# Optimization experiments

Hardware: AMD Instinct MI355X
Metric: run time of the kernel (lower is better)

## Reference

```python
import jax, jax.numpy as jnp
import numpy as np

RMAX = 5.0   # max_radius
NB = 8       # bessel bases
NSH = 9      # (lmax+1)^2, lmax=2
S = 4        # message passing steps


def _rms(x):
    return x * jax.lax.rsqrt(jnp.mean(x * x, axis=-1, keepdims=True) + 1e-6)


def _mlp(x, w1, b1, w2, b2):
    # 2-layer MLP (base_mlp_depth=2) with silu activation + rms_norm output
    return _rms(jax.nn.silu(x @ w1 + b1) @ w2 + b2)


def _sh(u):
    # real spherical harmonics up to l=2, component normalization (e3nn style), u: [E,3] unit vectors
    x, y, z = u[:, 0], u[:, 1], u[:, 2]
    s3, s5, s15 = 3.0 ** 0.5, 5.0 ** 0.5, 15.0 ** 0.5
    return jnp.stack([
        jnp.ones_like(x),
        s3 * x, s3 * y, s3 * z,
        s15 * x * y, s15 * y * z, 0.5 * s5 * (3.0 * z * z - 1.0),
        s15 * x * z, 0.5 * s15 * (x * x - y * y)], axis=1)


def setup_inputs() -> dict:
    key = jax.random.key(0)
    ks = iter(jax.random.split(key, 64))
    N, E, D, H, L, BOND = 20000, 640000, 128, 256, 128, 16

    def w(shape, fan):
        return jax.random.normal(next(ks), shape, jnp.float32) / np.float32(np.sqrt(fan))

    return dict(
        pos=jax.random.normal(next(ks), (N, 3), jnp.float32),
        c_in=jnp.ones((1,), jnp.float32),
        atom_type_index=jax.random.randint(next(ks), (N,), 0, 20),
        atom_code_index=jax.random.randint(next(ks), (N,), 0, 10),
        residue_code_index=jax.random.randint(next(ks), (N,), 0, 25),
        residue_sequence_index=jnp.zeros((N,), jnp.int32),  # max_sequence_length=1
        senders=jax.random.randint(next(ks), (E,), 0, N),
        receivers=jax.random.randint(next(ks), (E,), 0, N),
        bond_mask=jax.random.randint(next(ks), (E,), 0, 2),
        emb_at=w((20, 32), 1.0), emb_ac=w((10, 32), 1.0),
        emb_rc=w((25, 32), 1.0), emb_ri=w((1, 32), 1.0),
        emb_bond=w((2, BOND), 1.0),
        nenc_w1=w((D, H), D), nenc_b1=jnp.zeros((H,), jnp.float32),
        nenc_w2=w((H, L), H), nenc_b2=jnp.zeros((L,), jnp.float32),
        eenc_w1=w((NB * NSH + BOND, H), NB * NSH + BOND), eenc_b1=jnp.zeros((H,), jnp.float32),
        eenc_w2=w((H, L), H), eenc_b2=jnp.zeros((L,), jnp.float32),
        msg_w1=w((S, 3 * L, H), 3 * L), msg_b1=jnp.zeros((S, H), jnp.float32),
        msg_w2=w((S, H, L), H), msg_b2=jnp.zeros((S, L), jnp.float32),
        gate_w=w((S, L, 1), L), gate_b=jnp.zeros((S, 1), jnp.float32),
        upd_w1=w((S, 2 * L, H), 2 * L), upd_b1=jnp.zeros((S, H), jnp.float32),
        upd_w2=w((S, H, L), H), upd_b2=jnp.zeros((S, L), jnp.float32),
        head_w1=w((L, H), L), head_b1=jnp.zeros((H,), jnp.float32),
        head_w2=w((H, 3), H), head_b2=jnp.zeros((3,), jnp.float32),
    )


def reference(pos, c_in, atom_type_index, atom_code_index, residue_code_index,
              residue_sequence_index, senders, receivers, bond_mask,
              emb_at, emb_ac, emb_rc, emb_ri, emb_bond,
              nenc_w1, nenc_b1, nenc_w2, nenc_b2,
              eenc_w1, eenc_b1, eenc_w2, eenc_b2,
              msg_w1, msg_b1, msg_w2, msg_b2, gate_w, gate_b,
              upd_w1, upd_b1, upd_w2, upd_b2,
              head_w1, head_b1, head_w2, head_b2):
    N = pos.shape[0]
    E = senders.shape[0]

    # --- update_features: embeddings + edge vectors ---
    node_emb = jnp.concatenate([
        emb_at[atom_type_index], emb_ac[atom_code_index],
        emb_rc[residue_code_index], emb_ri[residue_sequence_index]], axis=1)  # [N,128]
    bond_emb = emb_bond[bond_mask]                                            # [E,16]

    up = pos / c_in
    vec = up[senders] - up[receivers]                                         # [E,3]
    r = jnp.sqrt(jnp.sum(vec * vec, axis=-1) + 1e-12)                         # [E]
    u = vec / r[:, None]

    # Bessel RBF: sqrt(2/rmax) * sin(n*pi*r/rmax) / r
    n = jnp.arange(1, NB + 1, dtype=jnp.float32)
    rbf = jnp.sqrt(2.0 / RMAX) * jnp.sin(n[None, :] * jnp.pi * r[:, None] / RMAX) / r[:, None]
    # cosine distance cutoff envelope
    cut = 0.5 * (jnp.cos(jnp.pi * jnp.minimum(r, RMAX) / RMAX) + 1.0) * (r < RMAX)

    ylm = _sh(u)                                                              # [E,9]
    radial = (rbf[:, :, None] * ylm[:, None, :]).reshape(E, NB * NSH) * cut[:, None]

    # --- encoders ---
    h = _mlp(node_emb, nenc_w1, nenc_b1, nenc_w2, nenc_b2)                    # [N,L]
    e = _mlp(jnp.concatenate([radial, bond_emb], axis=1),
             eenc_w1, eenc_b1, eenc_w2, eenc_b2)                              # [E,L]

    # --- message passing: gather -> MLP -> sigmoid-gate * cutoff -> scatter ---
    for s in range(S):
        m = _mlp(jnp.concatenate([h[senders], h[receivers], e], axis=1),
                 msg_w1[s], msg_b1[s], msg_w2[s], msg_b2[s])                  # [E,L]
        g = jax.nn.sigmoid(m @ gate_w[s] + gate_b[s]) * cut[:, None]          # [E,1]
        agg = jax.ops.segment_sum(m * g, receivers, num_segments=N)           # [N,L]
        h = h + _mlp(jnp.concatenate([h, agg], axis=1),
                     upd_w1[s], upd_b1[s], upd_w2[s], upd_b2[s])
        e = e + m

    # --- head: predict per-node 3-vector ---
    return jax.nn.silu(h @ head_w1 + head_b1) @ head_w2 + head_b2             # [N,3]
```

## Files before the change

kernel.cpp:

```cpp
#include <hip/hip_runtime.h>
#include <hip/hip_bf16.h>
#include <math.h>


#define TILE   16
#define STRIDE 20

using short8 = __attribute__((ext_vector_type(8))) short;
using f32x4  = __attribute__((ext_vector_type(4))) float;

__device__ __forceinline__ float silu_f(float x) {
  return x / (1.0f + __expf(-x));
}
__device__ __forceinline__ unsigned short f2b(float x) {
  union { float f; unsigned u; } v; v.f = x;
  unsigned r = v.u + 0x7fffu + ((v.u >> 16) & 1u);
  return (unsigned short)(r >> 16);
}
__device__ __forceinline__ float b2f(unsigned short h) {
  union { unsigned u; float f; } v; v.u = ((unsigned)h) << 16;
  return v.f;
}

__global__ __launch_bounds__(256) void pack_w_kernel(
    const float* __restrict__ src, unsigned short* __restrict__ dst,
    int Kreal, int KS, int NF)
{
  const int N = NF * 16;
  const int total = NF * KS * 512;
  for (int idx = blockIdx.x * 256 + threadIdx.x; idx < total; idx += gridDim.x * 256) {
    const int nf  = idx / (KS * 512);
    const int rem = idx - nf * (KS * 512);
    const int kk  = rem >> 9;
    const int p   = rem & 511;
    const int l   = p >> 3, j = p & 7;
    const int c   = nf * 16 + (l & 15);
    const int k   = kk * 32 + ((l >> 4) << 3) + j;
    dst[idx] = (k < Kreal) ? f2b(src[(size_t)k * N + c]) : (unsigned short)0;
  }
}

template<int KS1>
__device__ __forceinline__ void mfma_l1_compute(const unsigned short* __restrict__ x1,
                                                const unsigned short* __restrict__ w1p,
                                                int tid, f32x4 acc[8])
{
  const int w  = tid >> 6;
  const int l  = tid & 63;
  const int lr = l & 15;
  const int lk = (l >> 4) << 3;
  const int RS = KS1 * 32;
  const f32x4 zz = {0.f, 0.f, 0.f, 0.f};
  #pragma unroll
  for (int i = 0; i < 8; ++i) acc[i] = zz;

  for (int kk = 0; kk < KS1; ++kk) {
    short8 af[2];
    #pragma unroll
    for (int mf = 0; mf < 2; ++mf) {
      const int r = mf * 16 + lr;
      const int k = kk * 32 + lk;
      af[mf] = *(const short8*)&x1[r * RS + ((((k >> 3) ^ (r & 7))) << 3)];
    }
    #pragma unroll
    for (int nf = 0; nf < 4; ++nf) {
      const int nfg = w * 4 + nf;
      const short8 bf = *(const short8*)&w1p[(size_t)(((nfg * KS1) + kk) * 64 + l) * 8];
      #pragma unroll
      for (int mf = 0; mf < 2; ++mf)
        acc[mf * 4 + nf] = __builtin_amdgcn_mfma_f32_16x16x32_bf16(af[mf], bf, acc[mf * 4 + nf], 0, 0, 0);
    }
  }
}

__device__ __forceinline__ void l1_store_silu(const f32x4 acc[8],
                                              const float* __restrict__ b1,
                                              unsigned short* __restrict__ hsm,
                                              int tid)
{
  const int w = tid >> 6, l = tid & 63, lr = l & 15;
  #pragma unroll
  for (int nf = 0; nf < 4; ++nf) {
    const int c = (w * 4 + nf) * 16 + lr;
    const float bias = b1[c];
    #pragma unroll
    for (int mf = 0; mf < 2; ++mf) {
      #pragma unroll
      for (int q = 0; q < 4; ++q) {
        const int r = mf * 16 + ((l >> 4) << 2) + q;
        const float v = silu_f(acc[mf * 4 + nf][q] + bias);
        hsm[r * 256 + (((c >> 3) ^ (r & 7)) << 3) + (c & 7)] = f2b(v);
      }
    }
  }
}

__device__ __forceinline__ void mfma_l2(const unsigned short* __restrict__ hsm,
                                        const unsigned short* __restrict__ w2p,
                                        const float* __restrict__ b2,
                                        int tid, f32x4 acc2[4])
{
  const int w  = tid >> 6;
  const int l  = tid & 63;
  const int lr = l & 15;
  const int lk = (l >> 4) << 3;
  const f32x4 zz = {0.f, 0.f, 0.f, 0.f};
  #pragma unroll
  for (int i = 0; i < 4; ++i) acc2[i] = zz;

  for (int kk = 0; kk < 8; ++kk) {
    short8 af[2];
    #pragma unroll
    for (int mf = 0; mf < 2; ++mf) {
      const int r = mf * 16 + lr;
      const int k = kk * 32 + lk;
      af[mf] = *(const short8*)&hsm[r * 256 + (((k >> 3) ^ (r & 7)) << 3)];
    }
    #pragma unroll
    for (int nf2 = 0; nf2 < 2; ++nf2) {
      const int nfg = w * 2 + nf2;
      const short8 bf = *(const short8*)&w2p[(size_t)(((nfg * 8) + kk) * 64 + l) * 8];
      #pragma unroll
      for (int mf = 0; mf < 2; ++mf)
        acc2[mf * 2 + nf2] = __builtin_amdgcn_mfma_f32_16x16x32_bf16(af[mf], bf, acc2[mf * 2 + nf2], 0, 0, 0);
    }
  }
  #pragma unroll
  for (int nf2 = 0; nf2 < 2; ++nf2) {
    const float bias = b2[(w * 2 + nf2) * 16 + lr];
    #pragma unroll
    for (int mf = 0; mf < 2; ++mf) {
      #pragma unroll
      for (int q = 0; q < 4; ++q) acc2[mf * 2 + nf2][q] += bias;
    }
  }
}

__device__ __forceinline__ void rms_reduce(const f32x4 acc2[4], float* rsum,
                                           int tid, float mval[2][2][4])
{
  const int l = tid & 63;
  #pragma unroll
  for (int mf = 0; mf < 2; ++mf) {
    #pragma unroll
    for (int q = 0; q < 4; ++q) {
      float s = acc2[mf * 2][q] * acc2[mf * 2][q]
              + acc2[mf * 2 + 1][q] * acc2[mf * 2 + 1][q];
      s += __shfl_xor(s, 1); s += __shfl_xor(s, 2);
      s += __shfl_xor(s, 4); s += __shfl_xor(s, 8);
      if ((l & 15) == 0)
        atomicAdd(&rsum[mf * 16 + ((l >> 4) << 2) + q], s);
    }
  }
  __syncthreads();
  #pragma unroll
  for (int mf = 0; mf < 2; ++mf) {
    #pragma unroll
    for (int q = 0; q < 4; ++q) {
      const int r = mf * 16 + ((l >> 4) << 2) + q;
      const float inv = rsqrtf(rsum[r] * (1.0f / 128.0f) + 1e-6f);
      #pragma unroll
      for (int nf2 = 0; nf2 < 2; ++nf2)
        mval[mf][nf2][q] = acc2[mf * 2 + nf2][q] * inv;
    }
  }
}

__global__ __launch_bounds__(256, 5) void edge_enc_mfma(
    const float* __restrict__ pos, const float* __restrict__ c_in,
    const int* __restrict__ snd, const int* __restrict__ rcv,
    const int* __restrict__ bnd, const float* __restrict__ embb,
    const unsigned short* __restrict__ w1p, const float* __restrict__ b1,
    const unsigned short* __restrict__ w2p, const float* __restrict__ b2,
    unsigned short* __restrict__ e_g, float* __restrict__ cutb, int E)
{
  __shared__ __align__(16) unsigned short smem[32 * 256];
  unsigned short* x1  = smem;
  unsigned short* hsm = smem;
  __shared__ float grbf[32][8];
  __shared__ float gylm[32][9];
  __shared__ float gcut[32];
  __shared__ int   gbond[32];
  __shared__ float rsum[32];
  const int tid = threadIdx.x;
  const int e0  = blockIdx.x * 32;

  if (tid < 32) {
    rsum[tid] = 0.f;
    const int ed = min(e0 + tid, E - 1);
    const int sa = snd[ed], ra = rcv[ed];
    const float ci = c_in[0];
    const float vx = (pos[sa * 3 + 0] - pos[ra * 3 + 0]) / ci;
    const float vy = (pos[sa * 3 + 1] - pos[ra * 3 + 1]) / ci;
    const float vz = (pos[sa * 3 + 2] - pos[ra * 3 + 2]) / ci;
    const float r  = sqrtf(vx * vx + vy * vy + vz * vz + 1e-12f);
    const float ir = 1.0f / r;
    const float ux = vx * ir, uy = vy * ir, uz = vz * ir;
    const float PI = 3.14159265358979323846f;
    const float pr = PI * r * 0.2f;
    const float c0 = 0.632455532033675866f;
    #pragma unroll
    for (int n = 0; n < 8; ++n)
      grbf[tid][n] = c0 * sinf((float)(n + 1) * pr) * ir;
    const float cv = 0.5f * (cosf(PI * fminf(r, 5.0f) * 0.2f) + 1.0f)
                   * (r < 5.0f ? 1.0f : 0.0f);
    gcut[tid] = cv;
    if (e0 + tid < E) cutb[e0 + tid] = cv;
    const float s3  = 1.7320508075688772f;
    const float s5  = 2.2360679774997896f;
    const float s15 = 3.8729833462074170f;
    gylm[tid][0] = 1.0f;
    gylm[tid][1] = s3 * ux; gylm[tid][2] = s3 * uy; gylm[tid][3] = s3 * uz;
    gylm[tid][4] = s15 * ux * uy; gylm[tid][5] = s15 * uy * uz;
    gylm[tid][6] = 0.5f * s5 * (3.0f * uz * uz - 1.0f);
    gylm[tid][7] = s15 * ux * uz;
    gylm[tid][8] = 0.5f * s15 * (ux * ux - uy * uy);
    gbond[tid] = bnd[ed];
  }
  __syncthreads();
  for (int i = tid; i < 32 * 16; i += 256) {
    const int r = i >> 4, g = i & 15;
    union { short8 v; unsigned short u[8]; } t;
    #pragma unroll
    for (int j = 0; j < 8; ++j) {
      const int k = g * 8 + j;
      float v;
      if (k < 72) { const int n = k / 9, mm = k - 9 * n; v = grbf[r][n] * gylm[r][mm] * gcut[r]; }
      else if (k < 88) v = embb[gbond[r] * 16 + (k - 72)];
      else v = 0.f;
      t.u[j] = f2b(v);
    }
    *(short8*)&x1[r * 128 + ((g ^ (r & 7)) << 3)] = t.v;
  }
  __syncthreads();
  f32x4 acc1[8];
  mfma_l1_compute<4>(x1, w1p, tid, acc1);
  __syncthreads();
  l1_store_silu(acc1, b1, hsm, tid);
  __syncthreads();
  f32x4 acc2[4];
  mfma_l2(hsm, w2p, b2, tid, acc2);
  float mval[2][2][4];
  rms_reduce(acc2, rsum, tid, mval);
  const int l = tid & 63, w = tid >> 6, lr = l & 15;
  #pragma unroll
  for (int mf = 0; mf < 2; ++mf) {
    #pragma unroll
    for (int q = 0; q < 4; ++q) {
      const int r = mf * 16 + ((l >> 4) << 2) + q;
      const int ed = e0 + r;
      if (ed < E) {
        #pragma unroll
        for (int nf2 = 0; nf2 < 2; ++nf2) {
          const int c2 = (w * 2 + nf2) * 16 + lr;
          e_g[(size_t)ed * 128 + c2] = f2b(mval[mf][nf2][q]);
        }
      }
    }
  }
}

__global__ __launch_bounds__(256, 5) void msg_mfma(
    const unsigned short* __restrict__ hb, unsigned short* __restrict__ e_g,
    float* __restrict__ agg, const float* __restrict__ cutb,
    const int* __restrict__ snd, const int* __restrict__ rcv,
    const unsigned short* __restrict__ w1p, const float* __restrict__ b1,
    const unsigned short* __restrict__ w2p, const float* __restrict__ b2,
    const float* __restrict__ gw, const float* __restrict__ gb, int E)
{
  __shared__ __align__(16) unsigned short smem[32 * 384];
  unsigned short* x1  = smem;
  unsigned short* hsm = smem;
  __shared__ int   snd_s[32], rcv_s[32];
  __shared__ float cut_s[32];
  __shared__ float rsum[32], gsum[32];
  const int tid = threadIdx.x;
  const int e0  = blockIdx.x * 32;

  if (tid < 32) {
    rsum[tid] = 0.f; gsum[tid] = 0.f;
    const int ed = min(e0 + tid, E - 1);
    snd_s[tid] = snd[ed]; rcv_s[tid] = rcv[ed]; cut_s[tid] = cutb[ed];
  }
  __syncthreads();
  for (int i = tid; i < 32 * 48; i += 256) {
    const int r = i / 48, g = i - r * 48;
    short8 t;
    if (g < 32) {
      const int node = (g < 16) ? snd_s[r] : rcv_s[r];
      t = *(const short8*)&hb[(size_t)node * 128 + (g & 15) * 8];
    } else {
      const int ed = min(e0 + r, E - 1);
      t = *(const short8*)&e_g[(size_t)ed * 128 + (g - 32) * 8];
    }
    *(short8*)&x1[r * 384 + ((g ^ (r & 7)) << 3)] = t;
  }
  __syncthreads();
  f32x4 acc1[8];
  mfma_l1_compute<12>(x1, w1p, tid, acc1);
  __syncthreads();
  l1_store_silu(acc1, b1, hsm, tid);
  __syncthreads();
  f32x4 acc2[4];
  mfma_l2(hsm, w2p, b2, tid, acc2);
  float mval[2][2][4];
  rms_reduce(acc2, rsum, tid, mval);

  const int l = tid & 63, w = tid >> 6, lr = l & 15;
  const float gw0 = gw[(w * 2 + 0) * 16 + lr];
  const float gw1 = gw[(w * 2 + 1) * 16 + lr];
  #pragma unroll
  for (int mf = 0; mf < 2; ++mf) {
    #pragma unroll
    for (int q = 0; q < 4; ++q) {
      float p = mval[mf][0][q] * gw0 + mval[mf][1][q] * gw1;
      p += __shfl_xor(p, 1); p += __shfl_xor(p, 2);
      p += __shfl_xor(p, 4); p += __shfl_xor(p, 8);
      if ((l & 15) == 0)
        atomicAdd(&gsum[mf * 16 + ((l >> 4) << 2) + q], p);
    }
  }
  __syncthreads();
  const float gbv = gb[0];
  #pragma unroll
  for (int mf = 0; mf < 2; ++mf) {
    #pragma unroll
    for (int q = 0; q < 4; ++q) {
      const int r = mf * 16 + ((l >> 4) << 2) + q;
      const int ed = e0 + r;
      if (ed < E) {
        const float gr = cut_s[r] / (1.0f + __expf(-(gsum[r] + gbv)));
        const int rv = rcv_s[r];
        #pragma unroll
        for (int nf2 = 0; nf2 < 2; ++nf2) {
          const int c2 = (w * 2 + nf2) * 16 + lr;
          const float m = mval[mf][nf2][q];
          const float eo = b2f(e_g[(size_t)ed * 128 + c2]);
          e_g[(size_t)ed * 128 + c2] = f2b(eo + m);
          atomicAdd(&agg[(size_t)rv * 128 + c2], m * gr);
        }
      }
    }
  }
}

__global__ __launch_bounds__(256, 5) void upd_mfma(
    float* __restrict__ h, unsigned short* __restrict__ hb,
    const float* __restrict__ agg,
    const unsigned short* __restrict__ w1p, const float* __restrict__ b1,
    const unsigned short* __restrict__ w2p, const float* __restrict__ b2,
    int N)
{
  __shared__ __align__(16) unsigned short smem[32 * 256];
  unsigned short* x1  = smem;
  unsigned short* hsm = smem;
  __shared__ float rsum[32];
  const int tid = threadIdx.x;
  const int n0  = blockIdx.x * 32;
  if (tid < 32) rsum[tid] = 0.f;
  __syncthreads();
  for (int i = tid; i < 32 * 32; i += 256) {
    const int r = i >> 5, g = i & 31;
    const int n = min(n0 + r, N - 1);
    short8 t;
    if (g < 16) {
      t = *(const short8*)&hb[(size_t)n * 128 + g * 8];
    } else {
      const float4 f0 = *(const float4*)&agg[(size_t)n * 128 + (g - 16) * 8];
      const float4 f1 = *(const float4*)&agg[(size_t)n * 128 + (g - 16) * 8 + 4];
      union { short8 v; unsigned short u[8]; } tt;
      tt.u[0] = f2b(f0.x); tt.u[1] = f2b(f0.y); tt.u[2] = f2b(f0.z); tt.u[3] = f2b(f0.w);
      tt.u[4] = f2b(f1.x); tt.u[5] = f2b(f1.y); tt.u[6] = f2b(f1.z); tt.u[7] = f2b(f1.w);
      t = tt.v;
    }
    *(short8*)&x1[r * 256 + ((g ^ (r & 7)) << 3)] = t;
  }
  __syncthreads();
  f32x4 acc1[8];
  mfma_l1_compute<8>(x1, w1p, tid, acc1);
  __syncthreads();
  l1_store_silu(acc1, b1, hsm, tid);
  __syncthreads();
  f32x4 acc2[4];
  mfma_l2(hsm, w2p, b2, tid, acc2);
  float mval[2][2][4];
  rms_reduce(acc2, rsum, tid, mval);
  const int l = tid & 63, w = tid >> 6, lr = l & 15;
  #pragma unroll
  for (int mf = 0; mf < 2; ++mf) {
    #pragma unroll
    for (int q = 0; q < 4; ++q) {
      const int r = mf * 16 + ((l >> 4) << 2) + q;
      const int n = n0 + r;
      if (n < N) {
        #pragma unroll
        for (int nf2 = 0; nf2 < 2; ++nf2) {
          const int c2 = (w * 2 + nf2) * 16 + lr;
          const float nh = h[(size_t)n * 128 + c2] + mval[mf][nf2][q];
          h[(size_t)n * 128 + c2]  = nh;
          hb[(size_t)n * 128 + c2] = f2b(nh);
        }
      }
    }
  }
}


__device__ __forceinline__ float loadE(const float* p)          { return *p; }
__device__ __forceinline__ float loadE(const __hip_bfloat16* p) { return __bfloat162float(*p); }
__device__ __forceinline__ void  storeE(float* p, float v)          { *p = v; }
__device__ __forceinline__ void  storeE(__hip_bfloat16* p, float v) { *p = __float2bfloat16(v); }

template<int K1>
__device__ __forceinline__ void layer1_silu(const float* __restrict__ xs,
                                            const float* __restrict__ w1,
                                            const float* __restrict__ b1,
                                            float* __restrict__ hs, int tid)
{
  const int jh = tid & 127;
  const int tp = tid >> 7;
  const int tbase = 8 * tp;
  float a[8] = {0,0,0,0,0,0,0,0};
  float b[8] = {0,0,0,0,0,0,0,0};
  const float* wp = w1 + jh;
  for (int k = 0; k < K1; ++k) {
    const float4 x0 = *(const float4*)&xs[k*STRIDE + tbase];
    const float4 x1 = *(const float4*)&xs[k*STRIDE + tbase + 4];
    const float wa = wp[k*256];
    const float wb = wp[k*256 + 128];
    a[0] = fmaf(x0.x, wa, a[0]); a[1] = fmaf(x0.y, wa, a[1]);
    a[2] = fmaf(x0.z, wa, a[2]); a[3] = fmaf(x0.w, wa, a[3]);
    a[4] = fmaf(x1.x, wa, a[4]); a[5] = fmaf(x1.y, wa, a[5]);
    a[6] = fmaf(x1.z, wa, a[6]); a[7] = fmaf(x1.w, wa, a[7]);
    b[0] = fmaf(x0.x, wb, b[0]); b[1] = fmaf(x0.y, wb, b[1]);
    b[2] = fmaf(x0.z, wb, b[2]); b[3] = fmaf(x0.w, wb, b[3]);
    b[4] = fmaf(x1.x, wb, b[4]); b[5] = fmaf(x1.y, wb, b[5]);
    b[6] = fmaf(x1.z, wb, b[6]); b[7] = fmaf(x1.w, wb, b[7]);
  }
  const float ba = b1[jh];
  const float bb = b1[jh + 128];
  float4 oa0, oa1, ob0, ob1;
  oa0.x = silu_f(a[0] + ba); oa0.y = silu_f(a[1] + ba);
  oa0.z = silu_f(a[2] + ba); oa0.w = silu_f(a[3] + ba);
  oa1.x = silu_f(a[4] + ba); oa1.y = silu_f(a[5] + ba);
  oa1.z = silu_f(a[6] + ba); oa1.w = silu_f(a[7] + ba);
  ob0.x = silu_f(b[0] + bb); ob0.y = silu_f(b[1] + bb);
  ob0.z = silu_f(b[2] + bb); ob0.w = silu_f(b[3] + bb);
  ob1.x = silu_f(b[4] + bb); ob1.y = silu_f(b[5] + bb);
  ob1.z = silu_f(b[6] + bb); ob1.w = silu_f(b[7] + bb);
  *(float4*)&hs[jh*STRIDE + tbase]           = oa0;
  *(float4*)&hs[jh*STRIDE + tbase + 4]       = oa1;
  *(float4*)&hs[(jh+128)*STRIDE + tbase]     = ob0;
  *(float4*)&hs[(jh+128)*STRIDE + tbase + 4] = ob1;
}

__device__ __forceinline__ void layer2_bias(const float* __restrict__ hs,
                                            const float* __restrict__ w2,
                                            const float* __restrict__ b2,
                                            int tid, float cA[4], float cB[4])
{
  const int dh = tid & 63;
  const int tq = tid >> 6;
  const int tbase = 4 * tq;
  cA[0]=cA[1]=cA[2]=cA[3]=0.0f;
  cB[0]=cB[1]=cB[2]=cB[3]=0.0f;
  const float* wp = w2 + dh;
  for (int k = 0; k < 256; ++k) {
    const float4 hv = *(const float4*)&hs[k*STRIDE + tbase];
    const float wa = wp[k*128];
    const float wb = wp[k*128 + 64];
    cA[0] = fmaf(hv.x, wa, cA[0]); cA[1] = fmaf(hv.y, wa, cA[1]);
    cA[2] = fmaf(hv.z, wa, cA[2]); cA[3] = fmaf(hv.w, wa, cA[3]);
    cB[0] = fmaf(hv.x, wb, cB[0]); cB[1] = fmaf(hv.y, wb, cB[1]);
    cB[2] = fmaf(hv.z, wb, cB[2]); cB[3] = fmaf(hv.w, wb, cB[3]);
  }
  const float b2a = b2[dh];
  const float b2b = b2[dh + 64];
  #pragma unroll
  for (int tt = 0; tt < 4; ++tt) { cA[tt] += b2a; cB[tt] += b2b; }
}

__device__ __forceinline__ void rms4(float cA[4], float cB[4])
{
  float s[4];
  #pragma unroll
  for (int tt = 0; tt < 4; ++tt) s[tt] = cA[tt]*cA[tt] + cB[tt]*cB[tt];
  #pragma unroll
  for (int off = 32; off; off >>= 1) {
    #pragma unroll
    for (int tt = 0; tt < 4; ++tt) s[tt] += __shfl_xor(s[tt], off);
  }
  #pragma unroll
  for (int tt = 0; tt < 4; ++tt) {
    const float inv = rsqrtf(s[tt] * (1.0f/128.0f) + 1e-6f);
    cA[tt] *= inv; cB[tt] *= inv;
  }
}

__global__ __launch_bounds__(256) void zero_kernel(float4* __restrict__ p, int n4)
{
  const int i = blockIdx.x * 256 + threadIdx.x;
  if (i < n4) p[i] = make_float4(0.f, 0.f, 0.f, 0.f);
}

__global__ __launch_bounds__(256) void node_enc_kernel(
    const int* __restrict__ ati, const int* __restrict__ aci,
    const int* __restrict__ rci, const int* __restrict__ rsi,
    const float* __restrict__ emb_at, const float* __restrict__ emb_ac,
    const float* __restrict__ emb_rc, const float* __restrict__ emb_ri,
    const float* __restrict__ w1, const float* __restrict__ b1,
    const float* __restrict__ w2, const float* __restrict__ b2,
    float* __restrict__ h, unsigned short* __restrict__ hb, int N)
{
  __shared__ __align__(16) float xs[128*STRIDE];
  __shared__ __align__(16) float hs[256*STRIDE];
  __shared__ int idx_s[4][TILE];
  const int tid = threadIdx.x;
  const int n0 = blockIdx.x * TILE;
  if (tid < TILE) {
    const int n = min(n0 + tid, N - 1);
    idx_s[0][tid] = ati[n]; idx_s[1][tid] = aci[n];
    idx_s[2][tid] = rci[n]; idx_s[3][tid] = rsi[n];
  }
  __syncthreads();
  for (int i = tid; i < TILE*128; i += 256) {
    const int t = i >> 7, k = i & 127;
    const int seg = k >> 5, kk = k & 31;
    const float* tab = (seg == 0) ? emb_at : (seg == 1) ? emb_ac
                     : (seg == 2) ? emb_rc : emb_ri;
    xs[k*STRIDE + t] = tab[idx_s[seg][t]*32 + kk];
  }
  __syncthreads();
  layer1_silu<128>(xs, w1, b1, hs, tid);
  __syncthreads();
  float cA[4], cB[4];
  layer2_bias(hs, w2, b2, tid, cA, cB);
  rms4(cA, cB);
  const int dh = tid & 63, tq = tid >> 6;
  #pragma unroll
  for (int tt = 0; tt < 4; ++tt) {
    const int n = n0 + 4*tq + tt;
    if (n < N) {
      h[(size_t)n*128 + dh]      = cA[tt];
      h[(size_t)n*128 + dh + 64] = cB[tt];
      if (hb) {
        hb[(size_t)n*128 + dh]      = f2b(cA[tt]);
        hb[(size_t)n*128 + dh + 64] = f2b(cB[tt]);
      }
    }
  }
}

template<typename ET>
__global__ __launch_bounds__(256) void edge_enc_kernel(
    const float* __restrict__ pos, const float* __restrict__ c_in,
    const int* __restrict__ snd, const int* __restrict__ rcv,
    const int* __restrict__ bnd, const float* __restrict__ emb_bond,
    const float* __restrict__ w1, const float* __restrict__ b1,
    const float* __restrict__ w2, const float* __restrict__ b2,
    ET* __restrict__ e, float* __restrict__ cutb, int E)
{
  __shared__ __align__(16) float xs[88*STRIDE];
  __shared__ __align__(16) float hs[256*STRIDE];
  __shared__ float grbf[TILE][8];
  __shared__ float gylm[TILE][9];
  __shared__ float gcut[TILE];
  __shared__ int   gbond[TILE];
  const int tid = threadIdx.x;
  const int e0 = blockIdx.x * TILE;
  if (tid < TILE) {
    const int ed = min(e0 + tid, E - 1);
    const int sa = snd[ed], ra = rcv[ed];
    const float ci = c_in[0];
    const float vx = (pos[sa*3+0] - pos[ra*3+0]) / ci;
    const float vy = (pos[sa*3+1] - pos[ra*3+1]) / ci;
    const float vz = (pos[sa*3+2] - pos[ra*3+2]) / ci;
    const float r  = sqrtf(vx*vx + vy*vy + vz*vz + 1e-12f);
    const float ir = 1.0f / r;
    const float ux = vx*ir, uy = vy*ir, uz = vz*ir;
    const float PI = 3.14159265358979323846f;
    const float pr = PI * r * 0.2f;
    const float c0 = 0.632455532033675866f;
    #pragma unroll
    for (int n = 0; n < 8; ++n)
      grbf[tid][n] = c0 * sinf((float)(n + 1) * pr) * ir;
    const float cv = 0.5f * (cosf(PI * fminf(r, 5.0f) * 0.2f) + 1.0f)
                   * (r < 5.0f ? 1.0f : 0.0f);
    gcut[tid] = cv;
    cutb[ed] = cv;
    const float s3  = 1.7320508075688772f;
    const float s5  = 2.2360679774997896f;
    const float s15 = 3.8729833462074170f;
    gylm[tid][0] = 1.0f;
    gylm[tid][1] = s3*ux; gylm[tid][2] = s3*uy; gylm[tid][3] = s3*uz;
    gylm[tid][4] = s15*ux*uy; gylm[tid][5] = s15*uy*uz;
    gylm[tid][6] = 0.5f*s5*(3.0f*uz*uz - 1.0f);
    gylm[tid][7] = s15*ux*uz;
    gylm[tid][8] = 0.5f*s15*(ux*ux - uy*uy);
    gbond[tid] = bnd[ed];
  }
  __syncthreads();
  for (int i = tid; i < TILE*88; i += 256) {
    const int t = i & 15, k = i >> 4;
    float v;
    if (k < 72) {
      const int n = k / 9, m = k - 9*n;
      v = grbf[t][n] * gylm[t][m] * gcut[t];
    } else {
      v = emb_bond[gbond[t]*16 + (k - 72)];
    }
    xs[k*STRIDE + t] = v;
  }
  __syncthreads();
  layer1_silu<88>(xs, w1, b1, hs, tid);
  __syncthreads();
  float cA[4], cB[4];
  layer2_bias(hs, w2, b2, tid, cA, cB);
  rms4(cA, cB);
  const int dh = tid & 63, tq = tid >> 6;
  #pragma unroll
  for (int tt = 0; tt < 4; ++tt) {
    const int ed = e0 + 4*tq + tt;
    if (ed < E) {
      storeE(&e[(size_t)ed*128 + dh],      cA[tt]);
      storeE(&e[(size_t)ed*128 + dh + 64], cB[tt]);
    }
  }
}

template<typename ET>
__global__ __launch_bounds__(256) void msg_kernel(
    const float* __restrict__ h, ET* __restrict__ e,
    float* __restrict__ agg, const float* __restrict__ cutb,
    const int* __restrict__ snd, const int* __restrict__ rcv,
    const float* __restrict__ w1, const float* __restrict__ b1,
    const float* __restrict__ w2, const float* __restrict__ b2,
    const float* __restrict__ gw, const float* __restrict__ gb,
    int E)
{
  __shared__ __align__(16) float xs[384*STRIDE];
  __shared__ __align__(16) float hs[256*STRIDE];
  __shared__ int   snd_s[TILE], rcv_s[TILE];
  __shared__ float cut_s[TILE];
  const int tid = threadIdx.x;
  const int e0 = blockIdx.x * TILE;
  if (tid < TILE) {
    const int ed = min(e0 + tid, E - 1);
    snd_s[tid] = snd[ed]; rcv_s[tid] = rcv[ed]; cut_s[tid] = cutb[ed];
  }
  __syncthreads();
  for (int i = tid; i < TILE*384; i += 256) {
    const int t = i / 384, k = i - t*384;
    float v;
    if (k < 128)      v = h[(size_t)snd_s[t]*128 + k];
    else if (k < 256) v = h[(size_t)rcv_s[t]*128 + (k - 128)];
    else {
      const int ed = min(e0 + t, E - 1);
      v = loadE(&e[(size_t)ed*128 + (k - 256)]);
    }
    xs[k*STRIDE + t] = v;
  }
  __syncthreads();
  layer1_silu<384>(xs, w1, b1, hs, tid);
  __syncthreads();
  float cA[4], cB[4];
  layer2_bias(hs, w2, b2, tid, cA, cB);
  rms4(cA, cB);
  const int dh = tid & 63, tq = tid >> 6;
  const float gwa = gw[dh], gwb = gw[dh + 64];
  const float gbv = gb[0];
  float gv[4];
  #pragma unroll
  for (int tt = 0; tt < 4; ++tt) gv[tt] = cA[tt]*gwa + cB[tt]*gwb;
  #pragma unroll
  for (int off = 32; off; off >>= 1) {
    #pragma unroll
    for (int tt = 0; tt < 4; ++tt) gv[tt] += __shfl_xor(gv[tt], off);
  }
  #pragma unroll
  for (int tt = 0; tt < 4; ++tt) {
    const int t = 4*tq + tt;
    const int ed = e0 + t;
    if (ed < E) {
      const float g = cut_s[t] / (1.0f + __expf(-(gv[tt] + gbv)));
      const float eoA = xs[(256 + dh)*STRIDE + t];
      const float eoB = xs[(256 + dh + 64)*STRIDE + t];
      storeE(&e[(size_t)ed*128 + dh],      eoA + cA[tt]);
      storeE(&e[(size_t)ed*128 + dh + 64], eoB + cB[tt]);
      const int rv = rcv_s[t];
      atomicAdd(&agg[(size_t)rv*128 + dh],      cA[tt]*g);
      atomicAdd(&agg[(size_t)rv*128 + dh + 64], cB[tt]*g);
    }
  }
}

__global__ __launch_bounds__(256) void upd_kernel(
    float* __restrict__ h, const float* __restrict__ agg,
    const float* __restrict__ w1, const float* __restrict__ b1,
    const float* __restrict__ w2, const float* __restrict__ b2,
    int N)
{
  __shared__ __align__(16) float xs[256*STRIDE];
  __shared__ __align__(16) float hs[256*STRIDE];
  const int tid = threadIdx.x;
  const int n0 = blockIdx.x * TILE;
  for (int i = tid; i < TILE*256; i += 256) {
    const int t = i >> 8, k = i & 255;
    const int n = min(n0 + t, N - 1);
    const float v = (k < 128) ? h[(size_t)n*128 + k]
                              : agg[(size_t)n*128 + (k - 128)];
    xs[k*STRIDE + t] = v;
  }
  __syncthreads();
  layer1_silu<256>(xs, w1, b1, hs, tid);
  __syncthreads();
  float cA[4], cB[4];
  layer2_bias(hs, w2, b2, tid, cA, cB);
  rms4(cA, cB);
  const int dh = tid & 63, tq = tid >> 6;
  #pragma unroll
  for (int tt = 0; tt < 4; ++tt) {
    const int t = 4*tq + tt;
    const int n = n0 + t;
    if (n < N) {
      h[(size_t)n*128 + dh]      = xs[dh*STRIDE + t] + cA[tt];
      h[(size_t)n*128 + dh + 64] = xs[(dh + 64)*STRIDE + t] + cB[tt];
    }
  }
}

__global__ __launch_bounds__(256) void head_kernel(
    const float* __restrict__ h,
    const float* __restrict__ w1, const float* __restrict__ b1,
    const float* __restrict__ w2, const float* __restrict__ b2,
    float* __restrict__ out, int N)
{
  __shared__ __align__(16) float xs[128*STRIDE];
  __shared__ __align__(16) float hs[256*STRIDE];
  const int tid = threadIdx.x;
  const int n0 = blockIdx.x * TILE;
  for (int i = tid; i < TILE*128; i += 256) {
    const int t = i >> 7, k = i & 127;
    const int n = min(n0 + t, N - 1);
    xs[k*STRIDE + t] = h[(size_t)n*128 + k];
  }
  __syncthreads();
  layer1_silu<128>(xs, w1, b1, hs, tid);
  __syncthreads();
  if (tid < 48) {
    const int t = tid / 3, o = tid - 3*(tid/3);
    float acc = b2[o];
    for (int k = 0; k < 256; ++k)
      acc = fmaf(hs[k*STRIDE + t], w2[k*3 + o], acc);
    const int n = n0 + t;
    if (n < N) out[(size_t)n*3 + o] = acc;
  }
}

extern "C" void kernel_launch(void* const* d_in, const int* in_sizes, int n_in,
                              void* d_out, int out_size, void* d_ws, size_t ws_size,
                              hipStream_t stream)
{
  const float* pos      = (const float*)d_in[0];
  const float* c_in     = (const float*)d_in[1];
  const int*   ati      = (const int*)d_in[2];
  const int*   aci      = (const int*)d_in[3];
  const int*   rci      = (const int*)d_in[4];
  const int*   rsi      = (const int*)d_in[5];
  const int*   snd      = (const int*)d_in[6];
  const int*   rcv      = (const int*)d_in[7];
  const int*   bnd      = (const int*)d_in[8];
  const float* emb_at   = (const float*)d_in[9];
  const float* emb_ac   = (const float*)d_in[10];
  const float* emb_rc   = (const float*)d_in[11];
  const float* emb_ri   = (const float*)d_in[12];
  const float* emb_bond = (const float*)d_in[13];
  const float* nenc_w1  = (const float*)d_in[14];
  const float* nenc_b1  = (const float*)d_in[15];
  const float* nenc_w2  = (const float*)d_in[16];
  const float* nenc_b2  = (const float*)d_in[17];
  const float* eenc_w1  = (const float*)d_in[18];
  const float* eenc_b1  = (const float*)d_in[19];
  const float* eenc_w2  = (const float*)d_in[20];
  const float* eenc_b2  = (const float*)d_in[21];
  const float* msg_w1   = (const float*)d_in[22];
  const float* msg_b1   = (const float*)d_in[23];
  const float* msg_w2   = (const float*)d_in[24];
  const float* msg_b2   = (const float*)d_in[25];
  const float* gate_w   = (const float*)d_in[26];
  const float* gate_b   = (const float*)d_in[27];
  const float* upd_w1   = (const float*)d_in[28];
  const float* upd_b1   = (const float*)d_in[29];
  const float* upd_w2   = (const float*)d_in[30];
  const float* upd_b2   = (const float*)d_in[31];
  const float* head_w1  = (const float*)d_in[32];
  const float* head_b1  = (const float*)d_in[33];
  const float* head_w2  = (const float*)d_in[34];
  const float* head_b2  = (const float*)d_in[35];

  const int N = in_sizes[0] / 3;
  const int E = in_sizes[6];

  char* ws = (char*)d_ws;
  float* hbuf           = (float*)ws;           ws += (size_t)N * 128 * sizeof(float);
  unsigned short* hbb   = (unsigned short*)ws;  ws += (size_t)N * 128 * sizeof(unsigned short);
  float* aggbuf         = (float*)ws;           ws += (size_t)N * 128 * sizeof(float);
  float* cutbuf         = (float*)ws;           ws += (size_t)E * sizeof(float);
  unsigned short* packs = (unsigned short*)ws;
  const size_t eenc_w1p_o = 0;
  const size_t eenc_w2p_o = eenc_w1p_o + 16*4*512;
  const size_t msg_w1p_o  = eenc_w2p_o + 8*8*512;
  const size_t msg_w2p_o  = msg_w1p_o + 4*(size_t)(16*12*512);
  const size_t upd_w1p_o  = msg_w2p_o + 4*(size_t)(8*8*512);
  const size_t upd_w2p_o  = upd_w1p_o + 4*(size_t)(16*8*512);
  const size_t packs_end  = upd_w2p_o + 4*(size_t)(8*8*512);
  ws += packs_end * sizeof(unsigned short);
  unsigned short* ebuf_mfma = (unsigned short*)ws;
  const size_t need_mfma = (size_t)(ws - (char*)d_ws) + (size_t)E * 128 * sizeof(unsigned short);

  const int nb_n16 = (N + TILE - 1) / TILE;
  const int n4     = N * 128 / 4;

  if (ws_size >= need_mfma) {
    const int nb_e32 = (E + 31) / 32;
    const int nb_n32 = (N + 31) / 32;

    pack_w_kernel<<<96, 256, 0, stream>>>(eenc_w1, packs + eenc_w1p_o, 88, 4, 16);
    pack_w_kernel<<<96, 256, 0, stream>>>(eenc_w2, packs + eenc_w2p_o, 256, 8, 8);
    for (int s = 0; s < 4; ++s) {
      pack_w_kernel<<<96, 256, 0, stream>>>(msg_w1 + (size_t)s*384*256,
          packs + msg_w1p_o + (size_t)s*16*12*512, 384, 12, 16);
      pack_w_kernel<<<96, 256, 0, stream>>>(msg_w2 + (size_t)s*256*128,
          packs + msg_w2p_o + (size_t)s*8*8*512, 256, 8, 8);
      pack_w_kernel<<<96, 256, 0, stream>>>(upd_w1 + (size_t)s*256*256,
          packs + upd_w1p_o + (size_t)s*16*8*512, 256, 8, 16);
      pack_w_kernel<<<96, 256, 0, stream>>>(upd_w2 + (size_t)s*256*128,
          packs + upd_w2p_o + (size_t)s*8*8*512, 256, 8, 8);
    }

    node_enc_kernel<<<nb_n16, 256, 0, stream>>>(
        ati, aci, rci, rsi, emb_at, emb_ac, emb_rc, emb_ri,
        nenc_w1, nenc_b1, nenc_w2, nenc_b2, hbuf, hbb, N);

    edge_enc_mfma<<<nb_e32, 256, 0, stream>>>(
        pos, c_in, snd, rcv, bnd, emb_bond,
        packs + eenc_w1p_o, eenc_b1, packs + eenc_w2p_o, eenc_b2,
        ebuf_mfma, cutbuf, E);

    for (int s = 0; s < 4; ++s) {
      zero_kernel<<<(n4 + 255) / 256, 256, 0, stream>>>((float4*)aggbuf, n4);
      msg_mfma<<<nb_e32, 256, 0, stream>>>(
          hbb, ebuf_mfma, aggbuf, cutbuf, snd, rcv,
          packs + msg_w1p_o + (size_t)s*16*12*512, msg_b1 + (size_t)s*256,
          packs + msg_w2p_o + (size_t)s*8*8*512,   msg_b2 + (size_t)s*128,
          gate_w + (size_t)s*128, gate_b + s, E);
      upd_mfma<<<nb_n32, 256, 0, stream>>>(
          hbuf, hbb, aggbuf,
          packs + upd_w1p_o + (size_t)s*16*8*512, upd_b1 + (size_t)s*256,
          packs + upd_w2p_o + (size_t)s*8*8*512,  upd_b2 + (size_t)s*128, N);
    }

    head_kernel<<<nb_n16, 256, 0, stream>>>(
        hbuf, head_w1, head_b1, head_w2, head_b2, (float*)d_out, N);
  } else {
    char* ws2 = (char*)d_ws;
    float* hbuf2   = (float*)ws2;   ws2 += (size_t)N * 128 * sizeof(float);
    float* aggbuf2 = (float*)ws2;   ws2 += (size_t)N * 128 * sizeof(float);
    float* cutbuf2 = (float*)ws2;   ws2 += (size_t)E * sizeof(float);
    __hip_bfloat16* ebuf = (__hip_bfloat16*)ws2;
    const int nb_e16 = (E + TILE - 1) / TILE;

    node_enc_kernel<<<nb_n16, 256, 0, stream>>>(
        ati, aci, rci, rsi, emb_at, emb_ac, emb_rc, emb_ri,
        nenc_w1, nenc_b1, nenc_w2, nenc_b2, hbuf2, (unsigned short*)nullptr, N);

    edge_enc_kernel<__hip_bfloat16><<<nb_e16, 256, 0, stream>>>(
        pos, c_in, snd, rcv, bnd, emb_bond,
        eenc_w1, eenc_b1, eenc_w2, eenc_b2, ebuf, cutbuf2, E);

    for (int s = 0; s < 4; ++s) {
      zero_kernel<<<(n4 + 255) / 256, 256, 0, stream>>>((float4*)aggbuf2, n4);
      msg_kernel<__hip_bfloat16><<<nb_e16, 256, 0, stream>>>(
          hbuf2, ebuf, aggbuf2, cutbuf2, snd, rcv,
          msg_w1 + (size_t)s * 384 * 256, msg_b1 + (size_t)s * 256,
          msg_w2 + (size_t)s * 256 * 128, msg_b2 + (size_t)s * 128,
          gate_w + (size_t)s * 128, gate_b + s, E);
      upd_kernel<<<nb_n16, 256, 0, stream>>>(
          hbuf2, aggbuf2,
          upd_w1 + (size_t)s * 256 * 256, upd_b1 + (size_t)s * 256,
          upd_w2 + (size_t)s * 256 * 128, upd_b2 + (size_t)s * 128, N);
    }

    head_kernel<<<nb_n16, 256, 0, stream>>>(
        hbuf2, head_w1, head_b1, head_w2, head_b2, (float*)d_out, N);
  }
}
```

Before: 2.463 ms.

## Load message-MLP A fragments directly from global, skipping LDS staging

The message kernel no longer stages the gathered [h_s, h_r, e] rows into a 32x384 shared-memory tile. Each lane now loads its MFMA A-fragments straight from the global h and e arrays through per-row pointers. This drops one barrier and shrinks LDS, so the occupancy hint is raised from 5 to 6 blocks. The f32-to-bf16 conversion also switches to the HIP intrinsic. The risk is redundant global loads, since each warp re-reads the same A data, and register pressure under the tighter launch bound.

Result: slower. 2.957 ms (+20.0%).

```diff
diff --git a/kernel.cpp b/kernel.cpp
--- a/kernel.cpp
+++ b/kernel.cpp
@@ -13,9 +13,9 @@
   return x / (1.0f + __expf(-x));
 }
 __device__ __forceinline__ unsigned short f2b(float x) {
-  union { float f; unsigned u; } v; v.f = x;
-  unsigned r = v.u + 0x7fffu + ((v.u >> 16) & 1u);
-  return (unsigned short)(r >> 16);
+  union { __hip_bfloat16 b; unsigned short u; } v;
+  v.b = __float2bfloat16(x);
+  return v.u;
 }
 __device__ __forceinline__ float b2f(unsigned short h) {
   union { unsigned u; float f; } v; v.u = ((unsigned)h) << 16;
@@ -260,7 +260,7 @@
   }
 }
 
-__global__ __launch_bounds__(256, 5) void msg_mfma(
+__global__ __launch_bounds__(256, 6) void msg_mfma(
     const unsigned short* __restrict__ hb, unsigned short* __restrict__ e_g,
     float* __restrict__ agg, const float* __restrict__ cutb,
     const int* __restrict__ snd, const int* __restrict__ rcv,
@@ -268,9 +268,7 @@
     const unsigned short* __restrict__ w2p, const float* __restrict__ b2,
     const float* __restrict__ gw, const float* __restrict__ gb, int E)
 {
-  __shared__ __align__(16) unsigned short smem[32 * 384];
-  unsigned short* x1  = smem;
-  unsigned short* hsm = smem;
+  __shared__ __align__(16) unsigned short hsm[32 * 256];
   __shared__ int   snd_s[32], rcv_s[32];
   __shared__ float cut_s[32];
   __shared__ float rsum[32], gsum[32];
@@ -283,22 +281,47 @@
     snd_s[tid] = snd[ed]; rcv_s[tid] = rcv[ed]; cut_s[tid] = cutb[ed];
   }
   __syncthreads();
-  for (int i = tid; i < 32 * 48; i += 256) {
-    const int r = i / 48, g = i - r * 48;
-    short8 t;
-    if (g < 32) {
-      const int node = (g < 16) ? snd_s[r] : rcv_s[r];
-      t = *(const short8*)&hb[(size_t)node * 128 + (g & 15) * 8];
-    } else {
-      const int ed = min(e0 + r, E - 1);
-      t = *(const short8*)&e_g[(size_t)ed * 128 + (g - 32) * 8];
-    }
-    *(short8*)&x1[r * 384 + ((g ^ (r & 7)) << 3)] = t;
-  }
-  __syncthreads();
+
+  const int w  = tid >> 6;
+  const int l  = tid & 63;
+  const int lr = l & 15;
+  const int lk = (l >> 4) << 3;
+
+  const unsigned short* aS[2];
+  const unsigned short* aR[2];
+  const unsigned short* aE[2];
+  #pragma unroll
+  for (int mf = 0; mf < 2; ++mf) {
+    const int row = mf * 16 + lr;
+    aS[mf] = hb  + (size_t)snd_s[row] * 128 + lk;
+    aR[mf] = hb  + (size_t)rcv_s[row] * 128 + lk;
+    aE[mf] = e_g + (size_t)min(e0 + row, E - 1) * 128 + lk;
+  }
+
   f32x4 acc1[8];
-  mfma_l1_compute<12>(x1, w1p, tid, acc1);
-  __syncthreads();
+  const f32x4 zz = {0.f, 0.f, 0.f, 0.f};
+  #pragma unroll
+  for (int i = 0; i < 8; ++i) acc1[i] = zz;
+
+  #pragma unroll
+  for (int kk = 0; kk < 12; ++kk) {
+    short8 af[2];
+    #pragma unroll
+    for (int mf = 0; mf < 2; ++mf) {
+      const unsigned short* p = (kk < 4) ? aS[mf] + kk * 32
+                              : (kk < 8) ? aR[mf] + (kk - 4) * 32
+                                         : aE[mf] + (kk - 8) * 32;
+      af[mf] = *(const short8*)p;
+    }
+    #pragma unroll
+    for (int nf = 0; nf < 4; ++nf) {
+      const short8 bf = *(const short8*)&w1p[(size_t)((((w * 4 + nf) * 12) + kk) * 64 + l) * 8];
+      #pragma unroll
+      for (int mf = 0; mf < 2; ++mf)
+        acc1[mf * 4 + nf] = __builtin_amdgcn_mfma_f32_16x16x32_bf16(af[mf], bf, acc1[mf * 4 + nf], 0, 0, 0);
+    }
+  }
+
   l1_store_silu(acc1, b1, hsm, tid);
   __syncthreads();
   f32x4 acc2[4];
@@ -306,7 +329,6 @@
   float mval[2][2][4];
   rms_reduce(acc2, rsum, tid, mval);
 
-  const int l = tid & 63, w = tid >> 6, lr = l & 15;
   const float gw0 = gw[(w * 2 + 0) * 16 + lr];
   const float gw1 = gw[(w * 2 + 1) * 16 + lr];
   #pragma unroll
```
